# Performance work log

Hardware: AMD Instinct MI355X
Metric: run time of the kernel (lower is better)

## Reference

```python
import jax, jax.numpy as jnp
import numpy as np
import math
from jax import lax

B, T, C = 32, 512, 256
NL, NH, FF = 2, 4, 1024
DH = C // NH
NFREQ = 64   # n_even//2 for d_model=256 (even dims interleave sin/cos)
N_ODD = 128  # odd dims carry learned ramp a*t+b
MIN_P, MAX_P = 4.0, 10000.0


def setup_inputs() -> dict:
    key = jax.random.key(0)
    ks = jax.random.split(key, 16)
    def nrm(k, shape, s=0.02):
        return (jax.random.normal(k, shape) * s).astype(jnp.float32)
    x = jax.random.normal(ks[0], (B, T, C), jnp.float32)
    # strictly increasing normalized timestamps
    dts = jax.random.uniform(ks[1], (B, T), jnp.float32) * 0.02 + 1e-3
    ts = jnp.cumsum(dts, axis=1)
    return {
        "x": x, "ts": ts,
        "gru_Wih": nrm(ks[2], (3 * C, C)), "gru_Whh": nrm(ks[3], (3 * C, C)),
        "gru_bih": jnp.zeros((3 * C,), jnp.float32), "gru_bhh": jnp.zeros((3 * C,), jnp.float32),
        "ode_W": nrm(ks[4], (C, 4 * C)), "ode_b": jnp.zeros((C,), jnp.float32),
        "norm_ode_g": jnp.ones((C,), jnp.float32), "norm_ode_b": jnp.zeros((C,), jnp.float32),
        "norm_gru_g": jnp.ones((C,), jnp.float32), "norm_gru_b": jnp.zeros((C,), jnp.float32),
        "film_W": nrm(ks[5], (2 * C, C)), "film_b": jnp.zeros((2 * C,), jnp.float32),
        "te_a": nrm(ks[6], (N_ODD,), 1.0), "te_b": nrm(ks[7], (N_ODD,), 0.1),
        "qkv_W": nrm(ks[8], (NL, 3 * C, C)), "qkv_b": jnp.zeros((NL, 3 * C), jnp.float32),
        "out_W": nrm(ks[9], (NL, C, C)), "out_b": jnp.zeros((NL, C), jnp.float32),
        "ln1_g": jnp.ones((NL, C), jnp.float32), "ln1_b": jnp.zeros((NL, C), jnp.float32),
        "ln2_g": jnp.ones((NL, C), jnp.float32), "ln2_b": jnp.zeros((NL, C), jnp.float32),
        "ff1_W": nrm(ks[10], (NL, FF, C)), "ff1_b": jnp.zeros((NL, FF), jnp.float32),
        "ff2_W": nrm(ks[11], (NL, C, FF)), "ff2_b": jnp.zeros((NL, C), jnp.float32),
        "lnf_g": jnp.ones((C,), jnp.float32), "lnf_b": jnp.zeros((C,), jnp.float32),
    }


def _ln(x, g, b, eps=1e-5):
    m = x.mean(-1, keepdims=True)
    v = ((x - m) ** 2).mean(-1, keepdims=True)
    return (x - m) / jnp.sqrt(v + eps) * g + b


def _forward(x, ts, gru_Wih, gru_Whh, gru_bih, gru_bhh, ode_W, ode_b,
             norm_ode_g, norm_ode_b, norm_gru_g, norm_gru_b, film_W, film_b,
             te_a, te_b, qkv_W, qkv_b, out_W, out_b, ln1_g, ln1_b, ln2_g, ln2_b,
             ff1_W, ff1_b, ff2_W, ff2_b, lnf_g, lnf_b):
    Bx, Tx, Cx = x.shape

    def gru(xi, h):  # PyTorch GRUCell math
        gi = xi @ gru_Wih.T + gru_bih
        gh = h @ gru_Whh.T + gru_bhh
        ir, iz, inn = jnp.split(gi, 3, -1)
        hr, hz, hn = jnp.split(gh, 3, -1)
        r = jax.nn.sigmoid(ir + hr)
        z = jax.nn.sigmoid(iz + hz)
        n = jnp.tanh(inn + r * hn)
        return (1.0 - z) * n + z * h

    def step(h, inp):  # RK4 ODE jump + GRU jump per event
        xi, xp, dt = inp  # (B,C),(B,C),(B,1)
        dx = (xi - xp) / dt
        def f(hh):
            return jnp.tanh(jnp.concatenate([hh, xi, xp, dx], -1) @ ode_W.T + ode_b)
        k1 = f(h)
        k2 = f(h + 0.5 * dt * k1)
        k3 = f(h + 0.5 * dt * k2)
        k4 = f(h + dt * k3)
        h = h + dt / 6.0 * (k1 + 2.0 * k2 + 2.0 * k3 + k4)
        h = _ln(h, norm_ode_g, norm_ode_b)
        h = _ln(gru(xi, h), norm_gru_g, norm_gru_b)
        return h, h

    h0 = _ln(gru(x[:, 0], jnp.zeros((Bx, Cx), x.dtype)), norm_gru_g, norm_gru_b)
    xs = (x[:, 1:].swapaxes(0, 1), x[:, :-1].swapaxes(0, 1),
          (ts[:, 1:] - ts[:, :-1])[..., None].swapaxes(0, 1))
    _, ys = lax.scan(step, h0, xs)
    h = jnp.concatenate([h0[None], ys], 0).swapaxes(0, 1)  # (B,T,C)

    # FiLM params from hidden states
    gb = jax.nn.silu(h) @ film_W.T + film_b
    gamma, beta = jnp.split(gb, 2, -1)

    # TimeHybridEncoding: even dims interleaved sin/cos, odd dims learned ramp
    freqs = jnp.exp(-jnp.linspace(0.0, math.log(MAX_P / MIN_P), NFREQ)) * (2.0 * math.pi / MIN_P)
    phase = ts[..., None] * freqs  # (B,T,NFREQ)
    sc = jnp.stack([jnp.sin(phase), jnp.cos(phase)], -1).reshape(Bx, Tx, 2 * NFREQ)
    ramp = ts[..., None] * te_a + te_b  # (B,T,N_ODD)
    tme = jnp.zeros((Bx, Tx, Cx), x.dtype)
    tme = tme.at[..., 0::2].set(sc).at[..., 1::2].set(ramp)
    tme = (1.0 + gamma) * tme + beta

    # Pre-LN TransformerEncoder (eval mode: dropout off), relu FFN, final LN
    H = h + tme
    scale = 1.0 / jnp.sqrt(jnp.float32(DH))
    for l in range(NL):
        a = _ln(H, ln1_g[l], ln1_b[l])
        qkv = a @ qkv_W[l].T + qkv_b[l]
        q, k, v = jnp.split(qkv, 3, -1)
        q = q.reshape(Bx, Tx, NH, DH).transpose(0, 2, 1, 3)
        k = k.reshape(Bx, Tx, NH, DH).transpose(0, 2, 1, 3)
        v = v.reshape(Bx, Tx, NH, DH).transpose(0, 2, 1, 3)
        att = jax.nn.softmax(jnp.einsum('bhqd,bhkd->bhqk', q, k) * scale, axis=-1)
        o = jnp.einsum('bhqk,bhkd->bhqd', att, v).transpose(0, 2, 1, 3).reshape(Bx, Tx, Cx)
        H = H + o @ out_W[l].T + out_b[l]
        f2 = _ln(H, ln2_g[l], ln2_b[l])
        H = H + jax.nn.relu(f2 @ ff1_W[l].T + ff1_b[l]) @ ff2_W[l].T + ff2_b[l]
    return _ln(H, lnf_g, lnf_b)


def reference(x, ts, gru_Wih, gru_Whh, gru_bih, gru_bhh, ode_W, ode_b,
              norm_ode_g, norm_ode_b, norm_gru_g, norm_gru_b, film_W, film_b,
              te_a, te_b, qkv_W, qkv_b, out_W, out_b, ln1_g, ln1_b, ln2_g, ln2_b,
              ff1_W, ff1_b, ff2_W, ff2_b, lnf_g, lnf_b):
    return _forward(x, ts, gru_Wih, gru_Whh, gru_bih, gru_bhh, ode_W, ode_b,
                    norm_ode_g, norm_ode_b, norm_gru_g, norm_gru_b, film_W, film_b,
                    te_a, te_b, qkv_W, qkv_b, out_W, out_b, ln1_g, ln1_b, ln2_g, ln2_b,
                    ff1_W, ff1_b, ff2_W, ff2_b, lnf_g, lnf_b)
```

## Files before the change

kernel.cpp:

```cpp
#include <hip/hip_runtime.h>
#include <hip/hip_bf16.h>
#include <math.h>

typedef long long i64;

__device__ __forceinline__ float2 blockSum2_256(float a, float b, float* red) {
#pragma unroll
  for (int off = 32; off; off >>= 1) {
    a += __shfl_xor(a, off, 64);
    b += __shfl_xor(b, off, 64);
  }
  __syncthreads();
  if ((threadIdx.x & 63) == 0) {
    int w = threadIdx.x >> 6;
    red[w * 2 + 0] = a;
    red[w * 2 + 1] = b;
  }
  __syncthreads();
  return make_float2(red[0] + red[2] + red[4] + red[6],
                     red[1] + red[3] + red[5] + red[7]);
}

__device__ __forceinline__ float lnVal(float v, float g, float b, float* red) {
  float2 s = blockSum2_256(v, v * v, red);
  float mean = s.x * (1.0f / 256.0f);
  float var = s.y * (1.0f / 256.0f) - mean * mean;
  var = fmaxf(var, 0.0f);
  return (v - mean) * rsqrtf(var + 1e-5f) * g + b;
}

__device__ __forceinline__ void waveRed2d(double& a, double& b) {
#pragma unroll
  for (int off = 32; off; off >>= 1) {
    a += __shfl_xor(a, off, 64);
    b += __shfl_xor(b, off, 64);
  }
}

template <typename ACCT>
__global__ __launch_bounds__(256)
void gemm_nt_t(const float* __restrict__ A, int lda,
               const float* __restrict__ W, int ldw,
               const float* __restrict__ bias,
               const float* add,
               float* C, int ldc,
               int M, int N, int K, int relu)
{
  __shared__ float As[16][68];
  __shared__ float Ws[16][68];
  const int tid = threadIdx.x;
  const int tx = tid & 15, ty = tid >> 4;
  const int m0 = blockIdx.y * 64, n0 = blockIdx.x * 64;
  const int lrow = tid >> 2, lk = (tid & 3) << 2;
  ACCT acc[4][4] = {};
  for (int k0 = 0; k0 < K; k0 += 16) {
    float4 av = make_float4(0.f, 0.f, 0.f, 0.f);
    if (m0 + lrow < M) av = *(const float4*)(A + (i64)(m0 + lrow) * lda + k0 + lk);
    float4 wv = *(const float4*)(W + (i64)(n0 + lrow) * ldw + k0 + lk);
    As[lk + 0][lrow] = av.x; As[lk + 1][lrow] = av.y;
    As[lk + 2][lrow] = av.z; As[lk + 3][lrow] = av.w;
    Ws[lk + 0][lrow] = wv.x; Ws[lk + 1][lrow] = wv.y;
    Ws[lk + 2][lrow] = wv.z; Ws[lk + 3][lrow] = wv.w;
    __syncthreads();
#pragma unroll
    for (int kk = 0; kk < 16; ++kk) {
      ACCT a0 = (ACCT)As[kk][ty * 4 + 0], a1 = (ACCT)As[kk][ty * 4 + 1];
      ACCT a2 = (ACCT)As[kk][ty * 4 + 2], a3 = (ACCT)As[kk][ty * 4 + 3];
      ACCT b0 = (ACCT)Ws[kk][tx * 4 + 0], b1 = (ACCT)Ws[kk][tx * 4 + 1];
      ACCT b2 = (ACCT)Ws[kk][tx * 4 + 2], b3 = (ACCT)Ws[kk][tx * 4 + 3];
      acc[0][0] += a0 * b0; acc[0][1] += a0 * b1; acc[0][2] += a0 * b2; acc[0][3] += a0 * b3;
      acc[1][0] += a1 * b0; acc[1][1] += a1 * b1; acc[1][2] += a1 * b2; acc[1][3] += a1 * b3;
      acc[2][0] += a2 * b0; acc[2][1] += a2 * b1; acc[2][2] += a2 * b2; acc[2][3] += a2 * b3;
      acc[3][0] += a3 * b0; acc[3][1] += a3 * b1; acc[3][2] += a3 * b2; acc[3][3] += a3 * b3;
    }
    __syncthreads();
  }
#pragma unroll
  for (int i = 0; i < 4; ++i) {
    int m = m0 + ty * 4 + i;
    if (m >= M) continue;
#pragma unroll
    for (int j = 0; j < 4; ++j) {
      int n = n0 + tx * 4 + j;
      ACCT v = acc[i][j];
      if (bias) v += (ACCT)bias[n];
      if (relu) v = v > (ACCT)0 ? v : (ACCT)0;
      if (add) v += (ACCT)add[(i64)m * ldc + n];
      C[(i64)m * ldc + n] = (float)v;
    }
  }
}

__device__ __forceinline__ float siluf(float v) { return v / (1.0f + __expf(-v)); }

__global__ __launch_bounds__(256)
void gemm128(const float* __restrict__ A, int lda,
             const float* __restrict__ W, int ldw,
             const float* __restrict__ bias,
             const float* add,
             float* C, int ldc,
             int K, int relu, int silu_in)
{
  __shared__ float As[16][132];
  __shared__ float Ws[16][132];
  const int tid = threadIdx.x;
  const int tx = tid & 15, ty = tid >> 4;
  const int m0 = blockIdx.y * 128, n0 = blockIdx.x * 128;
  const int lrow = tid >> 1;
  const int lk = (tid & 1) * 8;
  float acc[8][8] = {};
  for (int k0 = 0; k0 < K; k0 += 16) {
    const float* ap = A + (i64)(m0 + lrow) * lda + k0 + lk;
    const float* wp = W + (i64)(n0 + lrow) * ldw + k0 + lk;
    float4 av0 = *(const float4*)(ap);
    float4 av1 = *(const float4*)(ap + 4);
    float4 wv0 = *(const float4*)(wp);
    float4 wv1 = *(const float4*)(wp + 4);
    if (silu_in) {
      av0.x = siluf(av0.x); av0.y = siluf(av0.y); av0.z = siluf(av0.z); av0.w = siluf(av0.w);
      av1.x = siluf(av1.x); av1.y = siluf(av1.y); av1.z = siluf(av1.z); av1.w = siluf(av1.w);
    }
    __syncthreads();
    As[lk + 0][lrow] = av0.x; As[lk + 1][lrow] = av0.y;
    As[lk + 2][lrow] = av0.z; As[lk + 3][lrow] = av0.w;
    As[lk + 4][lrow] = av1.x; As[lk + 5][lrow] = av1.y;
    As[lk + 6][lrow] = av1.z; As[lk + 7][lrow] = av1.w;
    Ws[lk + 0][lrow] = wv0.x; Ws[lk + 1][lrow] = wv0.y;
    Ws[lk + 2][lrow] = wv0.z; Ws[lk + 3][lrow] = wv0.w;
    Ws[lk + 4][lrow] = wv1.x; Ws[lk + 5][lrow] = wv1.y;
    Ws[lk + 6][lrow] = wv1.z; Ws[lk + 7][lrow] = wv1.w;
    __syncthreads();
#pragma unroll
    for (int kk = 0; kk < 16; ++kk) {
      float4 a0 = *(const float4*)&As[kk][ty * 4];
      float4 a1 = *(const float4*)&As[kk][64 + ty * 4];
      float4 b0 = *(const float4*)&Ws[kk][tx * 4];
      float4 b1 = *(const float4*)&Ws[kk][64 + tx * 4];
      float a[8] = {a0.x, a0.y, a0.z, a0.w, a1.x, a1.y, a1.z, a1.w};
      float bb[8] = {b0.x, b0.y, b0.z, b0.w, b1.x, b1.y, b1.z, b1.w};
#pragma unroll
      for (int i = 0; i < 8; ++i)
#pragma unroll
        for (int j = 0; j < 8; ++j)
          acc[i][j] = fmaf(a[i], bb[j], acc[i][j]);
    }
  }
#pragma unroll
  for (int i = 0; i < 8; ++i) {
    int m = m0 + ((i < 4) ? (ty * 4 + i) : (64 + ty * 4 + (i - 4)));
#pragma unroll
    for (int g = 0; g < 2; ++g) {
      int n = n0 + g * 64 + tx * 4;
      float v[4];
#pragma unroll
      for (int j = 0; j < 4; ++j) {
        float vv = acc[i][g * 4 + j];
        if (bias) vv += bias[n + j];
        if (relu) vv = fmaxf(vv, 0.f);
        if (add) vv += add[(i64)m * ldc + n + j];
        v[j] = vv;
      }
      *(float4*)(C + (i64)m * ldc + n) = make_float4(v[0], v[1], v[2], v[3]);
    }
  }
}

__global__ __launch_bounds__(256)
void pack_weights(const float* __restrict__ odeW, const float* __restrict__ Whh,
                  float* __restrict__ W4h, float* __restrict__ W4hh)
{
  int idx = blockIdx.x * 256 + threadIdx.x;
  if (idx < 65536) {
    int j = idx >> 8, k = idx & 255;
    W4h[((k >> 2) << 10) + (j << 2) + (k & 3)] = odeW[j * 1024 + k];
  } else {
    int t = idx - 65536;
    int j3 = t >> 8, k = t & 255;
    W4hh[(k >> 2) * 3072 + (j3 << 2) + (k & 3)] = Whh[j3 * 256 + k];
  }
}

__global__ __launch_bounds__(256)
void pack_rowsums(const float* __restrict__ odeW, const float* __restrict__ Whh,
                  const float* __restrict__ ngg, const float* __restrict__ ngb,
                  const float* __restrict__ nog, const float* __restrict__ nob,
                  double* __restrict__ Sd)
{
  int r = blockIdx.x * 256 + threadIdx.x;
  if (r < 256) {
    double s1 = 0.0, s0 = 0.0;
    for (int k = 0; k < 256; ++k) {
      double w = (double)odeW[r * 1024 + k];
      s1 += w * (double)ngg[k];
      s0 += w * (double)ngb[k];
    }
    Sd[r] = s1; Sd[256 + r] = s0;
  } else {
    int j3 = r - 256;
    double s1 = 0.0, s0 = 0.0;
    for (int k = 0; k < 256; ++k) {
      double w = (double)Whh[j3 * 256 + k];
      s1 += w * (double)nog[k];
      s0 += w * (double)nob[k];
    }
    Sd[512 + j3] = s1; Sd[1280 + j3] = s0;
  }
}

__global__ __launch_bounds__(256)
void dx_kernel(const float* __restrict__ x, const float* __restrict__ ts,
               float* __restrict__ dx)
{
  i64 row = blockIdx.x;
  int c = threadIdx.x;
  int t = (int)(row & 511);
  float v = 0.0f;
  if (t > 0) {
    double dt = (double)ts[row] - (double)ts[row - 1];
    v = (float)(((double)x[row * 256 + c] - (double)x[(row - 1) * 256 + c]) / dt);
  }
  dx[row * 256 + c] = v;
}

__global__ __launch_bounds__(256)
void fill_kernel(float* __restrict__ out, float v)
{
  i64 i = (i64)blockIdx.x * 256 + threadIdx.x;
  out[i] = v;
}

__device__ __forceinline__ float dot64s(const float* __restrict__ W, int kq, int j,
                                        const float* __restrict__ v)
{
  float a0 = 0.f, a1 = 0.f, a2 = 0.f, a3 = 0.f;
#pragma unroll
  for (int m4 = 0; m4 < 16; ++m4) {
    float4 w = *(const float4*)(W + (((kq << 4) + m4) << 10) + (j << 2));
    float4 x = *(const float4*)(v + (m4 << 2));
    a0 = fmaf(w.x, x.x, a0); a1 = fmaf(w.y, x.y, a1);
    a2 = fmaf(w.z, x.z, a2); a3 = fmaf(w.w, x.w, a3);
  }
  return (a0 + a1) + (a2 + a3);
}

__global__ __launch_bounds__(1024, 4)
void scan_kernel(const float* __restrict__ gi, const float* __restrict__ u,
                 const float* __restrict__ ts,
                 const float* __restrict__ W4h, const float* __restrict__ W4hh,
                 const double* __restrict__ Sd,
                 const float* __restrict__ bhh,
                 const float* __restrict__ nog, const float* __restrict__ nob,
                 const float* __restrict__ ngg, const float* __restrict__ ngb,
                 float* __restrict__ hseq)
{
  const int b = blockIdx.x;
  const int t = threadIdx.x;
  const int j = t & 255;
  const int kq = t >> 8;
  const int kbase = kq << 6;
  const int lane = t & 63;
  const int quad = (t >> 6) & 3;
  const int jp = kbase | lane;

  __shared__ __align__(16) float  hraw2f[256];
  __shared__ __align__(16) double vr2[256];
  __shared__ __align__(16) float  kb[256];
  __shared__ __align__(16) float  scA[1024];
  __shared__ __align__(16) float  scB[1024];
  __shared__ __align__(16) double predd[3][1024];
  __shared__ double redv[8];
  __shared__ double redh[8];

  const double gng = (double)ngg[jp], gnb = (double)ngb[jp];
  const double gog = (double)nog[jp], gob = (double)nob[jp];
  const double bhr = (double)bhh[jp], bhz = (double)bhh[256 + jp], bhn = (double)bhh[512 + jp];
  const double sa1 = Sd[jp], sa0 = Sd[256 + jp];
  const double sg1r = Sd[512 + jp],  sg0r = Sd[1280 + jp];
  const double sg1z = Sd[768 + jp],  sg0z = Sd[1536 + jp];
  const double sg1n = Sd[1024 + jp], sg0n = Sd[1792 + jp];

  double hLN = 0.0, mg = 0.0, invg = 1.0;

  {
    const i64 row0 = (i64)b * 512;
    double ir = (double)gi[row0 * 768 + jp];
    double iz = (double)gi[row0 * 768 + 256 + jp];
    double inn = (double)gi[row0 * 768 + 512 + jp];
    double rr = 1.0 / (1.0 + exp(-(ir + bhr)));
    double zz = 1.0 / (1.0 + exp(-(iz + bhz)));
    double nn = tanh(inn + rr * bhn);
    double hg_raw = (1.0 - zz) * nn;
    hraw2f[jp] = (float)(gng * hg_raw);
    double sa = hg_raw, sb = hg_raw * hg_raw;
    waveRed2d(sa, sb);
    if (lane == 0 && quad == 0) { redh[kq * 2] = sa; redh[kq * 2 + 1] = sb; }
    __syncthreads();
    double S = redh[0] + redh[2] + redh[4] + redh[6];
    double Q = redh[1] + redh[3] + redh[5] + redh[7];
    mg = S * (1.0 / 256.0);
    double var = Q * (1.0 / 256.0) - mg * mg;
    var = var > 0.0 ? var : 0.0;
    invg = 1.0 / sqrt(var + 1e-5);
    hLN = (hg_raw - mg) * invg * gng + gnb;
    if (quad == 0) hseq[row0 * 256 + jp] = (float)hLN;
    __syncthreads();
  }

  for (int s = 0; s < 511; ++s) {
    const double dt = (double)ts[b * 512 + s + 1] - (double)ts[b * 512 + s];
    const float dtf = (float)dt;
    const i64 row = (i64)(b * 512 + s + 1);

    const float u_j  = u[row * 256 + jp];
    const float ir2f = gi[row * 768 + jp];
    const float iz2f = gi[row * 768 + 256 + jp];
    const float in2f = gi[row * 768 + 512 + jp];

    scA[t] = dot64s(W4h, kq, j, hraw2f + kbase);
    __syncthreads();
    double psum = (double)(scA[jp] + scA[jp + 256] + scA[jp + 512] + scA[jp + 768]);
    double a_d = psum * invg - mg * invg * sa1 + sa0 + (double)u_j;
    float a_s = (float)a_d;
    float k1s = tanhf(a_s);
    kb[jp] = k1s;
    scB[t] = dot64s(W4h, kq, j, kb + kbase);
    __syncthreads();
    float bs2 = scB[jp] + scB[jp + 256] + scB[jp + 512] + scB[jp + 768];
    float k2s = tanhf(fmaf(0.5f * dtf, bs2, a_s));
    kb[jp] = k2s;
    scA[t] = dot64s(W4h, kq, j, kb + kbase);
    __syncthreads();
    float bs3 = scA[jp] + scA[jp + 256] + scA[jp + 512] + scA[jp + 768];
    float k3s = tanhf(fmaf(0.5f * dtf, bs3, a_s));
    kb[jp] = k3s;
    scB[t] = dot64s(W4h, kq, j, kb + kbase);
    __syncthreads();
    float bs4 = scB[jp] + scB[jp + 256] + scB[jp + 512] + scB[jp + 768];
    float k4s = tanhf(fmaf(dtf, bs4, a_s));
    double hode_raw = hLN + dt * (1.0 / 6.0) *
                      ((double)k1s + 2.0 * (double)k2s + 2.0 * (double)k3s + (double)k4s);
    vr2[jp] = gog * hode_raw;
    {
      double sa = hode_raw, sb = hode_raw * hode_raw;
      waveRed2d(sa, sb);
      if (lane == 0 && quad == 0) { redv[kq * 2] = sa; redv[kq * 2 + 1] = sb; }
    }
    {
      double g0 = 0.0, g1 = 0.0, g2 = 0.0;
#pragma unroll 2
      for (int m4 = 0; m4 < 16; ++m4) {
        const double2* hp = (const double2*)(vr2 + kbase + (m4 << 2));
        double2 ha = hp[0], hb2 = hp[1];
        const float* base = W4hh + ((kq << 4) + m4) * 3072 + (j << 2);
        float4 w0 = *(const float4*)(base);
        float4 w1 = *(const float4*)(base + 1024);
        float4 w2 = *(const float4*)(base + 2048);
        g0 += (double)w0.x * ha.x + (double)w0.y * ha.y + (double)w0.z * hb2.x + (double)w0.w * hb2.y;
        g1 += (double)w1.x * ha.x + (double)w1.y * ha.y + (double)w1.z * hb2.x + (double)w1.w * hb2.y;
        g2 += (double)w2.x * ha.x + (double)w2.y * ha.y + (double)w2.z * hb2.x + (double)w2.w * hb2.y;
      }
      predd[0][t] = g0; predd[1][t] = g1; predd[2][t] = g2;
    }
    __syncthreads();
    double hg_raw;
    {
      double mo = (redv[0] + redv[2] + redv[4] + redv[6]) * (1.0 / 256.0);
      double qo = (redv[1] + redv[3] + redv[5] + redv[7]) * (1.0 / 256.0);
      double var = qo - mo * mo; var = var > 0.0 ? var : 0.0;
      double invo = 1.0 / sqrt(var + 1e-5);
      double G0 = (predd[0][jp] + predd[0][jp + 256] + predd[0][jp + 512] + predd[0][jp + 768]) * invo
                  - mo * invo * sg1r + sg0r;
      double G1 = (predd[1][jp] + predd[1][jp + 256] + predd[1][jp + 512] + predd[1][jp + 768]) * invo
                  - mo * invo * sg1z + sg0z;
      double G2 = (predd[2][jp] + predd[2][jp + 256] + predd[2][jp + 512] + predd[2][jp + 768]) * invo
                  - mo * invo * sg1n + sg0n;
      double rr = 1.0 / (1.0 + exp(-((double)ir2f + G0 + bhr)));
      double zz = 1.0 / (1.0 + exp(-((double)iz2f + G1 + bhz)));
      double nn = tanh((double)in2f + rr * (G2 + bhn));
      double hodeLN = (hode_raw - mo) * invo * gog + gob;
      hg_raw = (1.0 - zz) * nn + zz * hodeLN;
      hraw2f[jp] = (float)(gng * hg_raw);
      double sa = hg_raw, sb = hg_raw * hg_raw;
      waveRed2d(sa, sb);
      if (lane == 0 && quad == 0) { redh[kq * 2] = sa; redh[kq * 2 + 1] = sb; }
    }
    __syncthreads();
    {
      double S = redh[0] + redh[2] + redh[4] + redh[6];
      double Q = redh[1] + redh[3] + redh[5] + redh[7];
      mg = S * (1.0 / 256.0);
      double var = Q * (1.0 / 256.0) - mg * mg;
      var = var > 0.0 ? var : 0.0;
      invg = 1.0 / sqrt(var + 1e-5);
      hLN = (hg_raw - mg) * invg * gng + gnb;
      if (quad == 0) hseq[row * 256 + jp] = (float)hLN;
    }
  }
}

__global__ __launch_bounds__(256)
void tme_kernel(const float* __restrict__ hseq, const float* __restrict__ gb,
                const float* __restrict__ ts,
                const float* __restrict__ te_a, const float* __restrict__ te_b,
                float* __restrict__ H)
{
  i64 idx = (i64)blockIdx.x * 256 + threadIdx.x;
  int c = (int)(idx & 255);
  i64 bt = idx >> 8;
  double tv = (double)ts[bt];
  double tme;
  if (c & 1) {
    int i = c >> 1;
    tme = tv * (double)te_a[i] + (double)te_b[i];
  } else {
    int f = c >> 2;
    double freq = exp(-(log(2500.0) / 63.0) * (double)f) * 1.5707963267948966;
    double ph = tv * freq;
    tme = ((c >> 1) & 1) ? cos(ph) : sin(ph);
  }
  float gamma = gb[bt * 512 + c];
  float beta = gb[bt * 512 + 256 + c];
  H[idx] = hseq[idx] + (1.0f + gamma) * (float)tme + beta;
}

__global__ __launch_bounds__(256)
void ln256_f32(const float* __restrict__ in, const float* __restrict__ g,
               const float* __restrict__ b, float* __restrict__ out)
{
  __shared__ float red[8];
  i64 row = blockIdx.x;
  float v = in[row * 256 + threadIdx.x];
  out[row * 256 + threadIdx.x] = lnVal(v, g[threadIdx.x], b[threadIdx.x], red);
}

__global__ __launch_bounds__(256)
void attn_kernel(const float* __restrict__ qkv, float* __restrict__ O)
{
  __shared__ float Qs[32][68];
  __shared__ float Ks[64][68];
  __shared__ float Vs[64][68];
  int bid = blockIdx.x;
  int qb = bid & 15, bh = bid >> 4;
  int h = bh & 3, b = bh >> 2;
  int tid = threadIdx.x;
  int r = tid >> 3, dg = tid & 7;
  int lane = tid & 63;
  int q0 = qb * 32;
  i64 base = (i64)b * 512 * 768;
  {
    int rr = tid >> 3, c8 = (tid & 7) * 8;
    const float* src = qkv + base + (i64)(q0 + rr) * 768 + h * 64 + c8;
    *(float4*)&Qs[rr][c8] = *(const float4*)src;
    *(float4*)&Qs[rr][c8 + 4] = *(const float4*)(src + 4);
  }
  float m = -1e30f, l = 0.0f;
  float o[8] = {0.f, 0.f, 0.f, 0.f, 0.f, 0.f, 0.f, 0.f};
  for (int kt = 0; kt < 8; ++kt) {
    __syncthreads();
    {
      int kr = tid >> 2, c16 = (tid & 3) * 16;
      const float* srcK = qkv + base + (i64)(kt * 64 + kr) * 768 + 256 + h * 64 + c16;
      const float* srcV = srcK + 256;
#pragma unroll
      for (int ii = 0; ii < 4; ++ii) {
        *(float4*)&Ks[kr][c16 + ii * 4] = *(const float4*)(srcK + ii * 4);
        *(float4*)&Vs[kr][c16 + ii * 4] = *(const float4*)(srcV + ii * 4);
      }
    }
    __syncthreads();
    float s[8] = {0.f, 0.f, 0.f, 0.f, 0.f, 0.f, 0.f, 0.f};
#pragma unroll
    for (int d4 = 0; d4 < 16; ++d4) {
      float4 qv = *(const float4*)&Qs[r][d4 * 4];
#pragma unroll
      for (int i = 0; i < 8; ++i) {
        float4 kv = *(const float4*)&Ks[dg * 8 + i][d4 * 4];
        s[i] += qv.x * kv.x + qv.y * kv.y + qv.z * kv.z + qv.w * kv.w;
      }
    }
    float ms = -1e30f;
#pragma unroll
    for (int i = 0; i < 8; ++i) { s[i] *= 0.125f; ms = fmaxf(ms, s[i]); }
    ms = fmaxf(ms, __shfl_xor(ms, 1, 64));
    ms = fmaxf(ms, __shfl_xor(ms, 2, 64));
    ms = fmaxf(ms, __shfl_xor(ms, 4, 64));
    float mnew = fmaxf(m, ms);
    float p[8];
    float ls = 0.0f;
#pragma unroll
    for (int i = 0; i < 8; ++i) { p[i] = __expf(s[i] - mnew); ls += p[i]; }
    ls += __shfl_xor(ls, 1, 64);
    ls += __shfl_xor(ls, 2, 64);
    ls += __shfl_xor(ls, 4, 64);
    float alpha = __expf(m - mnew);
    l = l * alpha + ls;
#pragma unroll
    for (int i = 0; i < 8; ++i) o[i] *= alpha;
    m = mnew;
#pragma unroll
    for (int i = 0; i < 8; ++i) {
#pragma unroll
      for (int dgk = 0; dgk < 8; ++dgk) {
        float pv = __shfl(p[i], (lane & 56) | dgk, 64);
        int kk = dgk * 8 + i;
        float4 v0 = *(const float4*)&Vs[kk][dg * 8];
        float4 v1 = *(const float4*)&Vs[kk][dg * 8 + 4];
        o[0] += pv * v0.x; o[1] += pv * v0.y; o[2] += pv * v0.z; o[3] += pv * v0.w;
        o[4] += pv * v1.x; o[5] += pv * v1.y; o[6] += pv * v1.z; o[7] += pv * v1.w;
      }
    }
  }
  float invl = 1.0f / l;
  float* dst = O + (i64)(b * 512 + q0 + r) * 256 + h * 64 + dg * 8;
  float4 r0 = make_float4(o[0] * invl, o[1] * invl, o[2] * invl, o[3] * invl);
  float4 r1 = make_float4(o[4] * invl, o[5] * invl, o[6] * invl, o[7] * invl);
  *(float4*)dst = r0;
  *(float4*)(dst + 4) = r1;
}

extern "C" void kernel_launch(void* const* d_in, const int* in_sizes, int n_in,
                              void* d_out, int out_size, void* d_ws, size_t ws_size,
                              hipStream_t stream)
{
  (void)in_sizes; (void)n_in; (void)out_size;
  const float* x       = (const float*)d_in[0];
  const float* ts      = (const float*)d_in[1];
  const float* gru_Wih = (const float*)d_in[2];
  const float* gru_Whh = (const float*)d_in[3];
  const float* gru_bih = (const float*)d_in[4];
  const float* gru_bhh = (const float*)d_in[5];
  const float* ode_W   = (const float*)d_in[6];
  const float* ode_b   = (const float*)d_in[7];
  const float* nog     = (const float*)d_in[8];
  const float* nob     = (const float*)d_in[9];
  const float* ngg     = (const float*)d_in[10];
  const float* ngb     = (const float*)d_in[11];
  const float* film_W  = (const float*)d_in[12];
  const float* film_b  = (const float*)d_in[13];
  const float* te_a    = (const float*)d_in[14];
  const float* te_bb   = (const float*)d_in[15];
  const float* qkv_W   = (const float*)d_in[16];
  const float* qkv_b   = (const float*)d_in[17];
  const float* out_W   = (const float*)d_in[18];
  const float* out_b   = (const float*)d_in[19];
  const float* ln1_g   = (const float*)d_in[20];
  const float* ln1_b   = (const float*)d_in[21];
  const float* ln2_g   = (const float*)d_in[22];
  const float* ln2_b   = (const float*)d_in[23];
  const float* ff1_W   = (const float*)d_in[24];
  const float* ff1_b   = (const float*)d_in[25];
  const float* ff2_W   = (const float*)d_in[26];
  const float* ff2_b   = (const float*)d_in[27];
  const float* lnf_g   = (const float*)d_in[28];
  const float* lnf_b   = (const float*)d_in[29];

  const size_t NEED = 25432064ull * 4ull;
  if (ws_size < NEED) {
    fill_kernel<<<16384, 256, 0, stream>>>((float*)d_out, 1000.0f);
    return;
  }
  float*  ws   = (float*)d_ws;
  float*  W4h  = ws;
  float*  W4hh = ws + 65536;
  double* Sd   = (double*)(ws + 262144);
  float*  SA   = ws + 266240;
  float*  SB   = ws + 4460544;
  float*  Hb   = ws + 8654848;
  float*  BIG  = ws + 12849152;

  float* u = SA;   float* aln = SA;  float* f2 = SA;
  float* dxb = SB; float* hseq = SB; float* Obuf = SB; float* ff1o = SB;
  float* gi = BIG; float* gb = BIG;  float* qkvb = BIG;

  const int MROW = 32 * 512;

  pack_weights<<<1024, 256, 0, stream>>>(ode_W, gru_Whh, W4h, W4hh);
  pack_rowsums<<<4, 256, 0, stream>>>(ode_W, gru_Whh, ngg, ngb, nog, nob, Sd);
  dx_kernel<<<MROW, 256, 0, stream>>>(x, ts, dxb);
  gemm_nt_t<double><<<dim3(12, 256), 256, 0, stream>>>(x, 256, gru_Wih, 256, gru_bih,
                                                       nullptr, gi, 768, MROW, 768, 256, 0);
  gemm_nt_t<double><<<dim3(4, 256), 256, 0, stream>>>(x + 256, 256, ode_W + 256, 1024, ode_b,
                                                      nullptr, u + 256, 256, MROW - 1, 256, 256, 0);
  gemm_nt_t<double><<<dim3(4, 256), 256, 0, stream>>>(x, 256, ode_W + 512, 1024, nullptr,
                                                      u + 256, u + 256, 256, MROW - 1, 256, 256, 0);
  gemm_nt_t<double><<<dim3(4, 256), 256, 0, stream>>>(dxb + 256, 256, ode_W + 768, 1024, nullptr,
                                                      u + 256, u + 256, 256, MROW - 1, 256, 256, 0);
  scan_kernel<<<32, 1024, 0, stream>>>(gi, u, ts, W4h, W4hh, Sd, gru_bhh,
                                       nog, nob, ngg, ngb, hseq);
  gemm128<<<dim3(4, 128), 256, 0, stream>>>(hseq, 256, film_W, 256, film_b, nullptr,
                                            gb, 512, 256, 0, 1);
  tme_kernel<<<MROW, 256, 0, stream>>>(hseq, gb, ts, te_a, te_bb, Hb);

  for (int l = 0; l < 2; ++l) {
    ln256_f32<<<MROW, 256, 0, stream>>>(Hb, ln1_g + 256 * l, ln1_b + 256 * l, aln);
    gemm128<<<dim3(6, 128), 256, 0, stream>>>(aln, 256, qkv_W + (i64)196608 * l, 256,
                                              qkv_b + 768 * l, nullptr,
                                              qkvb, 768, 256, 0, 0);
    attn_kernel<<<2048, 256, 0, stream>>>(qkvb, Obuf);
    gemm128<<<dim3(2, 128), 256, 0, stream>>>(Obuf, 256, out_W + (i64)65536 * l, 256,
                                              out_b + 256 * l, Hb, Hb, 256, 256, 0, 0);
    ln256_f32<<<MROW, 256, 0, stream>>>(Hb, ln2_g + 256 * l, ln2_b + 256 * l, f2);
    for (int c = 0; c < 4; ++c) {
      const int r0 = c * 4096;
      gemm128<<<dim3(8, 32), 256, 0, stream>>>(f2 + (i64)r0 * 256, 256,
                                               ff1_W + (i64)262144 * l, 256,
                                               ff1_b + 1024 * l, nullptr,
                                               ff1o, 1024, 256, 1, 0);
      gemm_nt_t<float><<<dim3(4, 64), 256, 0, stream>>>(ff1o, 1024,
                                                        ff2_W + (i64)262144 * l, 1024,
                                                        ff2_b + 256 * l,
                                                        Hb + (i64)r0 * 256, Hb + (i64)r0 * 256, 256,
                                                        4096, 256, 1024, 0);
    }
  }
  ln256_f32<<<MROW, 256, 0, stream>>>(Hb, lnf_g, lnf_b, (float*)d_out);
}
```

Measured before the change: 10.61 ms.

## Shrink scan kernel to 256 threads, each computing full dot products

The sequential GRU-ODE scan block drops from 1024 threads (4-way split-K over the hidden dimension plus shared-memory partial-sum reduction) to 256 threads that each compute whole 256-long dot products. This removes the partial-sum scratch buffers and one reduction barrier per RK4 stage, and uses double-buffered k vectors so fewer barriers are needed. In exchange each thread does four times the serial FMA and weight-load work per step, with less latency hiding from a quarter of the waves.

Measured after the change: 17.89 ms. +68.6%, slower.

```diff
diff --git a/kernel.cpp b/kernel.cpp
--- a/kernel.cpp
+++ b/kernel.cpp
@@ -229,21 +229,50 @@
   out[i] = v;
 }
 
-__device__ __forceinline__ float dot64s(const float* __restrict__ W, int kq, int j,
+__device__ __forceinline__ float rk4dot(const float* __restrict__ W, int j,
                                         const float* __restrict__ v)
 {
-  float a0 = 0.f, a1 = 0.f, a2 = 0.f, a3 = 0.f;
-#pragma unroll
-  for (int m4 = 0; m4 < 16; ++m4) {
-    float4 w = *(const float4*)(W + (((kq << 4) + m4) << 10) + (j << 2));
-    float4 x = *(const float4*)(v + (m4 << 2));
-    a0 = fmaf(w.x, x.x, a0); a1 = fmaf(w.y, x.y, a1);
-    a2 = fmaf(w.z, x.z, a2); a3 = fmaf(w.w, x.w, a3);
-  }
-  return (a0 + a1) + (a2 + a3);
-}
-
-__global__ __launch_bounds__(1024, 4)
+  float sl[4];
+#pragma unroll
+  for (int s = 0; s < 4; ++s) {
+    float a0 = 0.f, a1 = 0.f, a2 = 0.f, a3 = 0.f;
+#pragma unroll
+    for (int m = 0; m < 16; ++m) {
+      float4 w = *(const float4*)(W + (((s << 4) + m) << 10) + (j << 2));
+      float4 x = *(const float4*)(v + (s << 6) + (m << 2));
+      a0 = fmaf(w.x, x.x, a0); a1 = fmaf(w.y, x.y, a1);
+      a2 = fmaf(w.z, x.z, a2); a3 = fmaf(w.w, x.w, a3);
+    }
+    sl[s] = (a0 + a1) + (a2 + a3);
+  }
+  return ((sl[0] + sl[1]) + sl[2]) + sl[3];
+}
+
+__device__ __forceinline__ void grudot(const float* __restrict__ W4hh, int j,
+                                       const double* __restrict__ v,
+                                       double& G0, double& G1, double& G2)
+{
+  G0 = 0.0; G1 = 0.0; G2 = 0.0;
+#pragma unroll
+  for (int s = 0; s < 4; ++s) {
+    double g0 = 0.0, g1 = 0.0, g2 = 0.0;
+#pragma unroll 2
+    for (int m = 0; m < 16; ++m) {
+      const double2* hp = (const double2*)(v + (s << 6) + (m << 2));
+      double2 ha = hp[0], hb2 = hp[1];
+      const float* base = W4hh + ((s << 4) + m) * 3072 + (j << 2);
+      float4 w0 = *(const float4*)(base);
+      float4 w1 = *(const float4*)(base + 1024);
+      float4 w2 = *(const float4*)(base + 2048);
+      g0 += (double)w0.x * ha.x + (double)w0.y * ha.y + (double)w0.z * hb2.x + (double)w0.w * hb2.y;
+      g1 += (double)w1.x * ha.x + (double)w1.y * ha.y + (double)w1.z * hb2.x + (double)w1.w * hb2.y;
+      g2 += (double)w2.x * ha.x + (double)w2.y * ha.y + (double)w2.z * hb2.x + (double)w2.w * hb2.y;
+    }
+    G0 += g0; G1 += g1; G2 += g2;
+  }
+}
+
+__global__ __launch_bounds__(256, 1)
 void scan_kernel(const float* __restrict__ gi, const float* __restrict__ u,
                  const float* __restrict__ ts,
                  const float* __restrict__ W4h, const float* __restrict__ W4hh,
@@ -254,46 +283,40 @@
                  float* __restrict__ hseq)
 {
   const int b = blockIdx.x;
-  const int t = threadIdx.x;
-  const int j = t & 255;
-  const int kq = t >> 8;
-  const int kbase = kq << 6;
-  const int lane = t & 63;
-  const int quad = (t >> 6) & 3;
-  const int jp = kbase | lane;
+  const int j = threadIdx.x;
+  const int lane = j & 63;
+  const int wv = j >> 6;
 
   __shared__ __align__(16) float  hraw2f[256];
   __shared__ __align__(16) double vr2[256];
-  __shared__ __align__(16) float  kb[256];
-  __shared__ __align__(16) float  scA[1024];
-  __shared__ __align__(16) float  scB[1024];
-  __shared__ __align__(16) double predd[3][1024];
+  __shared__ __align__(16) float  kbA[256];
+  __shared__ __align__(16) float  kbB[256];
   __shared__ double redv[8];
   __shared__ double redh[8];
 
-  const double gng = (double)ngg[jp], gnb = (double)ngb[jp];
-  const double gog = (double)nog[jp], gob = (double)nob[jp];
-  const double bhr = (double)bhh[jp], bhz = (double)bhh[256 + jp], bhn = (double)bhh[512 + jp];
-  const double sa1 = Sd[jp], sa0 = Sd[256 + jp];
-  const double sg1r = Sd[512 + jp],  sg0r = Sd[1280 + jp];
-  const double sg1z = Sd[768 + jp],  sg0z = Sd[1536 + jp];
-  const double sg1n = Sd[1024 + jp], sg0n = Sd[1792 + jp];
-
-  double hLN = 0.0, mg = 0.0, invg = 1.0;
+  const double gng = (double)ngg[j], gnb = (double)ngb[j];
+  const double gog = (double)nog[j], gob = (double)nob[j];
+  const double bhr = (double)bhh[j], bhz = (double)bhh[256 + j], bhn = (double)bhh[512 + j];
+  const double sa1 = Sd[j], sa0 = Sd[256 + j];
+  const double sg1r = Sd[512 + j],  sg0r = Sd[1280 + j];
+  const double sg1z = Sd[768 + j],  sg0z = Sd[1536 + j];
+  const double sg1n = Sd[1024 + j], sg0n = Sd[1792 + j];
+
+  double hLN, mg, invg;
 
   {
     const i64 row0 = (i64)b * 512;
-    double ir = (double)gi[row0 * 768 + jp];
-    double iz = (double)gi[row0 * 768 + 256 + jp];
-    double inn = (double)gi[row0 * 768 + 512 + jp];
+    double ir = (double)gi[row0 * 768 + j];
+    double iz = (double)gi[row0 * 768 + 256 + j];
+    double inn = (double)gi[row0 * 768 + 512 + j];
     double rr = 1.0 / (1.0 + exp(-(ir + bhr)));
     double zz = 1.0 / (1.0 + exp(-(iz + bhz)));
     double nn = tanh(inn + rr * bhn);
     double hg_raw = (1.0 - zz) * nn;
-    hraw2f[jp] = (float)(gng * hg_raw);
+    hraw2f[j] = (float)(gng * hg_raw);
     double sa = hg_raw, sb = hg_raw * hg_raw;
     waveRed2d(sa, sb);
-    if (lane == 0 && quad == 0) { redh[kq * 2] = sa; redh[kq * 2 + 1] = sb; }
+    if (lane == 0) { redh[wv * 2] = sa; redh[wv * 2 + 1] = sb; }
     __syncthreads();
     double S = redh[0] + redh[2] + redh[4] + redh[6];
     double Q = redh[1] + redh[3] + redh[5] + redh[7];
@@ -302,7 +325,7 @@
     var = var > 0.0 ? var : 0.0;
     invg = 1.0 / sqrt(var + 1e-5);
     hLN = (hg_raw - mg) * invg * gng + gnb;
-    if (quad == 0) hseq[row0 * 256 + jp] = (float)hLN;
+    hseq[row0 * 256 + j] = (float)hLN;
     __syncthreads();
   }
 
@@ -311,78 +334,53 @@
     const float dtf = (float)dt;
     const i64 row = (i64)(b * 512 + s + 1);
 
-    const float u_j  = u[row * 256 + jp];
-    const float ir2f = gi[row * 768 + jp];
-    const float iz2f = gi[row * 768 + 256 + jp];
-    const float in2f = gi[row * 768 + 512 + jp];
-
-    scA[t] = dot64s(W4h, kq, j, hraw2f + kbase);
-    __syncthreads();
-    double psum = (double)(scA[jp] + scA[jp + 256] + scA[jp + 512] + scA[jp + 768]);
-    double a_d = psum * invg - mg * invg * sa1 + sa0 + (double)u_j;
+    const float u_j  = u[row * 256 + j];
+    const float ir2f = gi[row * 768 + j];
+    const float iz2f = gi[row * 768 + 256 + j];
+    const float in2f = gi[row * 768 + 512 + j];
+
+    float p1 = rk4dot(W4h, j, hraw2f);
+    double a_d = (double)p1 * invg - mg * invg * sa1 + sa0 + (double)u_j;
     float a_s = (float)a_d;
     float k1s = tanhf(a_s);
-    kb[jp] = k1s;
-    scB[t] = dot64s(W4h, kq, j, kb + kbase);
-    __syncthreads();
-    float bs2 = scB[jp] + scB[jp + 256] + scB[jp + 512] + scB[jp + 768];
-    float k2s = tanhf(fmaf(0.5f * dtf, bs2, a_s));
-    kb[jp] = k2s;
-    scA[t] = dot64s(W4h, kq, j, kb + kbase);
-    __syncthreads();
-    float bs3 = scA[jp] + scA[jp + 256] + scA[jp + 512] + scA[jp + 768];
-    float k3s = tanhf(fmaf(0.5f * dtf, bs3, a_s));
-    kb[jp] = k3s;
-    scB[t] = dot64s(W4h, kq, j, kb + kbase);
-    __syncthreads();
-    float bs4 = scB[jp] + scB[jp + 256] + scB[jp + 512] + scB[jp + 768];
-    float k4s = tanhf(fmaf(dtf, bs4, a_s));
+    kbA[j] = k1s;
+    __syncthreads();
+    float k2s = tanhf(fmaf(0.5f * dtf, rk4dot(W4h, j, kbA), a_s));
+    kbB[j] = k2s;
+    __syncthreads();
+    float k3s = tanhf(fmaf(0.5f * dtf, rk4dot(W4h, j, kbB), a_s));
+    kbA[j] = k3s;
+    __syncthreads();
+    float k4s = tanhf(fmaf(dtf, rk4dot(W4h, j, kbA), a_s));
     double hode_raw = hLN + dt * (1.0 / 6.0) *
                       ((double)k1s + 2.0 * (double)k2s + 2.0 * (double)k3s + (double)k4s);
-    vr2[jp] = gog * hode_raw;
+    vr2[j] = gog * hode_raw;
     {
       double sa = hode_raw, sb = hode_raw * hode_raw;
       waveRed2d(sa, sb);
-      if (lane == 0 && quad == 0) { redv[kq * 2] = sa; redv[kq * 2 + 1] = sb; }
-    }
-    {
-      double g0 = 0.0, g1 = 0.0, g2 = 0.0;
-#pragma unroll 2
-      for (int m4 = 0; m4 < 16; ++m4) {
-        const double2* hp = (const double2*)(vr2 + kbase + (m4 << 2));
-        double2 ha = hp[0], hb2 = hp[1];
-        const float* base = W4hh + ((kq << 4) + m4) * 3072 + (j << 2);
-        float4 w0 = *(const float4*)(base);
-        float4 w1 = *(const float4*)(base + 1024);
-        float4 w2 = *(const float4*)(base + 2048);
-        g0 += (double)w0.x * ha.x + (double)w0.y * ha.y + (double)w0.z * hb2.x + (double)w0.w * hb2.y;
-        g1 += (double)w1.x * ha.x + (double)w1.y * ha.y + (double)w1.z * hb2.x + (double)w1.w * hb2.y;
-        g2 += (double)w2.x * ha.x + (double)w2.y * ha.y + (double)w2.z * hb2.x + (double)w2.w * hb2.y;
-      }
-      predd[0][t] = g0; predd[1][t] = g1; predd[2][t] = g2;
+      if (lane == 0) { redv[wv * 2] = sa; redv[wv * 2 + 1] = sb; }
     }
     __syncthreads();
     double hg_raw;
     {
+      double G0, G1, G2;
+      grudot(W4hh, j, vr2, G0, G1, G2);
       double mo = (redv[0] + redv[2] + redv[4] + redv[6]) * (1.0 / 256.0);
       double qo = (redv[1] + redv[3] + redv[5] + redv[7]) * (1.0 / 256.0);
       double var = qo - mo * mo; var = var > 0.0 ? var : 0.0;
       double invo = 1.0 / sqrt(var + 1e-5);
-      double G0 = (predd[0][jp] + predd[0][jp + 256] + predd[0][jp + 512] + predd[0][jp + 768]) * invo
-                  - mo * invo * sg1r + sg0r;
-      double G1 = (predd[1][jp] + predd[1][jp + 256] + predd[1][jp + 512] + predd[1][jp + 768]) * invo
-                  - mo * invo * sg1z + sg0z;
-      double G2 = (predd[2][jp] + predd[2][jp + 256] + predd[2][jp + 512] + predd[2][jp + 768]) * invo
-                  - mo * invo * sg1n + sg0n;
+      G0 = G0 * invo - mo * invo * sg1r + sg0r;
+      G1 = G1 * invo - mo * invo * sg1z + sg0z;
+      G2 = G2 * invo - mo * invo * sg1n + sg0n;
       double rr = 1.0 / (1.0 + exp(-((double)ir2f + G0 + bhr)));
       double zz = 1.0 / (1.0 + exp(-((double)iz2f + G1 + bhz)));
       double nn = tanh((double)in2f + rr * (G2 + bhn));
       double hodeLN = (hode_raw - mo) * invo * gog + gob;
       hg_raw = (1.0 - zz) * nn + zz * hodeLN;
-      hraw2f[jp] = (float)(gng * hg_raw);
+      hraw2f[j] = (float)(gng * hg_raw);
       double sa = hg_raw, sb = hg_raw * hg_raw;
       waveRed2d(sa, sb);
-      if (lane == 0 && quad == 0) { redh[kq * 2] = sa; redh[kq * 2 + 1] = sb; }
+      if (lane == 0) { redh[wv * 2] = sa; redh[wv * 2 + 1] = sb; }
     }
     __syncthreads();
     {
@@ -393,7 +391,7 @@
       var = var > 0.0 ? var : 0.0;
       invg = 1.0 / sqrt(var + 1e-5);
       hLN = (hg_raw - mg) * invg * gng + gnb;
-      if (quad == 0) hseq[row * 256 + jp] = (float)hLN;
+      hseq[row * 256 + j] = (float)hLN;
     }
   }
 }
@@ -585,8 +583,8 @@
                                                       u + 256, u + 256, 256, MROW - 1, 256, 256, 0);
   gemm_nt_t<double><<<dim3(4, 256), 256, 0, stream>>>(dxb + 256, 256, ode_W + 768, 1024, nullptr,
                                                       u + 256, u + 256, 256, MROW - 1, 256, 256, 0);
-  scan_kernel<<<32, 1024, 0, stream>>>(gi, u, ts, W4h, W4hh, Sd, gru_bhh,
-                                       nog, nob, ngg, ngb, hseq);
+  scan_kernel<<<32, 256, 0, stream>>>(gi, u, ts, W4h, W4hh, Sd, gru_bhh,
+                                      nog, nob, ngg, ngb, hseq);
   gemm128<<<dim3(4, 128), 256, 0, stream>>>(hseq, 256, film_W, 256, film_b, nullptr,
                                             gb, 512, 256, 0, 1);
   tme_kernel<<<MROW, 256, 0, stream>>>(hseq, gb, ts, te_a, te_bb, Hb);
```
